# Optimization experiments

Hardware: AMD Instinct MI355X
Metric: run time of the kernel (lower is better)

The kernel has to match this reference:

```python
import jax, jax.numpy as jnp
import numpy as np

NUM_HEADS = 8
NEG_SLOPE = 0.2


def setup_inputs() -> dict:
    key = jax.random.key(0)
    k1, k2, k3, k4 = jax.random.split(key, 4)
    B, N, D_IN, D_K, D_V = 4, 4096, 256, 256, 256
    x = jax.random.normal(k1, (B, N, D_IN), dtype=jnp.float32)
    Wq = jax.random.normal(k2, (D_IN, D_K), dtype=jnp.float32) * (1.0 / np.sqrt(D_IN))
    Wk = jax.random.normal(k3, (D_IN, D_K), dtype=jnp.float32) * (1.0 / np.sqrt(D_IN))
    Wv = jax.random.normal(k4, (D_IN, D_V), dtype=jnp.float32) * (1.0 / np.sqrt(D_IN))
    return {"x": x, "Wq": Wq, "Wk": Wk, "Wv": Wv}


def reference(x, Wq, Wk, Wv):
    B, N, _ = x.shape
    nh = NUM_HEADS
    dim_k = Wq.shape[1]
    dim_v = Wv.shape[1]
    dk, dv = dim_k // nh, dim_v // nh
    nor_fact = 1.0 / np.sqrt(dk)
    # project and split heads: [B, H, N, dk]
    q = (x @ Wq).reshape(B, N, nh, dk).transpose(0, 2, 1, 3)
    k = (x @ Wk).reshape(B, N, nh, dk).transpose(0, 2, 1, 3)
    v = (x @ Wv).reshape(B, N, nh, dv).transpose(0, 2, 1, 3)
    # all-pairs scores, scaled then LeakyReLU (no softmax)
    dist = jnp.einsum('bhnd,bhmd->bhnm', q, k) * nor_fact
    dist = jnp.where(dist >= 0, dist, NEG_SLOPE * dist)
    att = jnp.einsum('bhnm,bhmd->bhnd', dist, v)
    return att.transpose(0, 2, 1, 3).reshape(B, N, dim_v)
```

## Files before the change

kernel.cpp:

```cpp
#include <hip/hip_runtime.h>

typedef __attribute__((ext_vector_type(8))) short short8;
typedef __attribute__((ext_vector_type(4))) float f32x4;
typedef __attribute__((ext_vector_type(2))) unsigned int u32x2;
typedef __attribute__((ext_vector_type(4))) unsigned int u32x4;

#define MFMA16x32(A, B, C) \
  __builtin_amdgcn_mfma_f32_16x16x32_bf16((A), (B), (C), 0, 0, 0)

__device__ __forceinline__ void async_cp16(const unsigned short* g, void* l) {
  __builtin_amdgcn_global_load_lds(
      (const __attribute__((address_space(1))) unsigned int*)g,
      (__attribute__((address_space(3))) unsigned int*)l, 16, 0, 0);
}

__device__ __forceinline__ unsigned int fbits(float f) {
  return __builtin_bit_cast(unsigned int, f);
}
__device__ __forceinline__ unsigned int pack_bf16(float a, float b) {
  return __builtin_amdgcn_perm(fbits(b), fbits(a), 0x07060302u);
}
__device__ __forceinline__ unsigned short bf16_rne(float f) {
  unsigned int u = fbits(f);
  return (unsigned short)((u + 0x8000u) >> 16);
}
__device__ __forceinline__ unsigned int relu_pk_bf16(unsigned int x) {
  unsigned int r;
  asm("v_pk_max_i16 %0, %1, 0" : "=v"(r) : "v"(x));
  return r;
}

__global__ __launch_bounds__(256) void prep_kernel(
    const float* __restrict__ x, unsigned short* __restrict__ xb,
    const float* __restrict__ Wq, const float* __restrict__ Wk,
    const float* __restrict__ Wv, unsigned short* __restrict__ WT) {
  __shared__ float tile[32][33];
  if (blockIdx.x < 4096) {
    const size_t i = ((size_t)blockIdx.x * 256 + threadIdx.x) * 4;
    const float4 f = *(const float4*)(x + i);
    u32x2 u = {(unsigned int)bf16_rne(f.x) | ((unsigned int)bf16_rne(f.y) << 16),
               (unsigned int)bf16_rne(f.z) | ((unsigned int)bf16_rne(f.w) << 16)};
    *(u32x2*)(xb + i) = u;
    return;
  }
  const int bid = blockIdx.x - 4096;
  const int g = bid / 64, rem = bid % 64;
  const int k0 = (rem >> 3) * 32, n0 = (rem & 7) * 32;
  const float* W = (g == 0) ? Wq : (g == 1) ? Wk : Wv;
  const int t = threadIdx.x;
  {
    const int kr = t >> 3, nc = (t & 7) * 4;
    const float4 f = *(const float4*)(W + (size_t)(k0 + kr) * 256 + n0 + nc);
    tile[kr][nc + 0] = f.x; tile[kr][nc + 1] = f.y;
    tile[kr][nc + 2] = f.z; tile[kr][nc + 3] = f.w;
  }
  __syncthreads();
  {
    const int nr = t >> 3, kc = (t & 7) * 4;
    unsigned int u0 = (unsigned int)bf16_rne(tile[kc + 0][nr]) |
                      ((unsigned int)bf16_rne(tile[kc + 1][nr]) << 16);
    unsigned int u1 = (unsigned int)bf16_rne(tile[kc + 2][nr]) |
                      ((unsigned int)bf16_rne(tile[kc + 3][nr]) << 16);
    u32x2 u = {u0, u1};
    *(u32x2*)(WT + (size_t)g * 65536 + (size_t)(n0 + nr) * 256 + k0 + kc) = u;
  }
}

__global__ __launch_bounds__(256, 2) void proj_kernel(
    const unsigned short* __restrict__ xb, const unsigned short* __restrict__ WT,
    unsigned short* __restrict__ QH, unsigned short* __restrict__ KH,
    unsigned short* __restrict__ VT) {
  __shared__ __align__(16) char smem[65536];
  const int tid = threadIdx.x;
  const int w = tid >> 6, lane = tid & 63, l15 = lane & 15, quad = lane >> 4;
  const int bid = blockIdx.x;
  const int mtile = bid / 6, nt = bid % 6;
  const int g = nt >> 1, n0 = (nt & 1) * 128;
  const int m0 = mtile * 128;

  const int srow = lane >> 3, useg = lane & 7;
  const int swz = (useg ^ srow) * 8;
  const unsigned short* aS = xb + (size_t)(m0 + w * 32 + srow) * 256 + swz;
  const unsigned short* bS =
      WT + (size_t)g * 65536 + (size_t)(n0 + w * 32 + srow) * 256 + swz;

#pragma unroll
  for (int j = 0; j < 4; j++) {
    async_cp16(aS + j * 2048, smem + w * 4096 + j * 1024);
    async_cp16(bS + j * 2048, smem + 16384 + w * 4096 + j * 1024);
  }
  __syncthreads();

  const f32x4 zero = {0.f, 0.f, 0.f, 0.f};
  f32x4 acc[2][8];
#pragma unroll
  for (int s = 0; s < 2; s++)
#pragma unroll
    for (int c = 0; c < 8; c++) acc[s][c] = zero;

  const int sw = l15 & 7;
  for (int t = 0; t < 4; t++) {
    const int nb = t & 1;
    const int kn = ((t + 1) & 3) * 64;
#pragma unroll
    for (int j = 0; j < 4; j++) {
      async_cp16(aS + kn + j * 2048,
                 smem + (nb ^ 1) * 32768 + w * 4096 + j * 1024);
      async_cp16(bS + kn + j * 2048,
                 smem + (nb ^ 1) * 32768 + 16384 + w * 4096 + j * 1024);
    }
    const char* Ab = smem + nb * 32768;
    const char* Bb = Ab + 16384;
#pragma unroll
    for (int ks = 0; ks < 2; ks++) {
      const int seg = ((ks * 4 + quad) ^ sw) * 16;
      short8 af[2], bf[8];
#pragma unroll
      for (int s = 0; s < 2; s++)
        af[s] = *(const short8*)(Ab + (w * 32 + s * 16 + l15) * 128 + seg);
#pragma unroll
      for (int c = 0; c < 8; c++)
        bf[c] = *(const short8*)(Bb + (c * 16 + l15) * 128 + seg);
      if (g < 2) {
#pragma unroll
        for (int s = 0; s < 2; s++)
#pragma unroll
          for (int c = 0; c < 8; c++)
            acc[s][c] = MFMA16x32(bf[c], af[s], acc[s][c]);
      } else {
#pragma unroll
        for (int s = 0; s < 2; s++)
#pragma unroll
          for (int c = 0; c < 8; c++)
            acc[s][c] = MFMA16x32(af[s], bf[c], acc[s][c]);
      }
    }
    __syncthreads();
  }

  if (g < 2) {
    unsigned short* O = g ? KH : QH;
    const float sc = g ? 1.0f : 0.17677669529663688f;
#pragma unroll
    for (int s = 0; s < 2; s++)
#pragma unroll
      for (int c = 0; c < 8; c++) {
        const int row = m0 + w * 32 + s * 16 + l15;
        const int col = n0 + c * 16 + quad * 4;
        const int bb = row >> 12, nn = row & 4095;
        const int hh = col >> 5, dl = col & 31;
        u32x2 pk = {pack_bf16(acc[s][c][0] * sc, acc[s][c][1] * sc),
                    pack_bf16(acc[s][c][2] * sc, acc[s][c][3] * sc)};
        *(u32x2*)(O + ((size_t)(bb * 8 + hh) * 4096 + nn) * 32 + dl) = pk;
      }
  } else {
#pragma unroll
    for (int s = 0; s < 2; s++)
#pragma unroll
      for (int c = 0; c < 8; c++) {
        const int col = n0 + c * 16 + l15;
        const int hh = col >> 5, dl = col & 31;
        const int row = m0 + w * 32 + s * 16 + quad * 4;
        const int bb = row >> 12;
        const int nn = (row & 4064) | (quad << 3) | ((s & 1) << 2);
        u32x2 pk = {pack_bf16(acc[s][c][0], acc[s][c][1]),
                    pack_bf16(acc[s][c][2], acc[s][c][3])};
        *(u32x2*)(VT + (size_t)((bb * 8 + hh) * 32 + dl) * 4096 + nn) = pk;
      }
  }
}

__global__ __launch_bounds__(512) void mkv_kernel(
    const unsigned short* __restrict__ KH, const unsigned short* __restrict__ VT,
    unsigned short* __restrict__ MW) {
  __shared__ __align__(16) float Mred[8][32][32];
  const int tid = threadIdx.x;
  const int w = tid >> 6, lane = tid & 63, l15 = lane & 15, quad = lane >> 4;
  const int bh = blockIdx.x;

  const f32x4 zero = {0.f, 0.f, 0.f, 0.f};
  f32x4 mm[2][2];
#pragma unroll
  for (int dt = 0; dt < 2; dt++)
#pragma unroll
    for (int it = 0; it < 2; it++) mm[dt][it] = zero;

  const unsigned short* Vg = VT + ((size_t)bh * 32 + l15) * 4096 + quad * 8;
  const unsigned short* Kg = KH + (size_t)bh * 4096 * 32;

  for (int g = 0; g < 16; g++) {
    const int kb = w * 512 + g * 32;
    short8 va[2];
#pragma unroll
    for (int dt = 0; dt < 2; dt++)
      va[dt] = *(const short8*)(Vg + (size_t)dt * 16 * 4096 + kb);
    short8 kv0, kv1;
#pragma unroll
    for (int j = 0; j < 8; j++) {
      const int key = kb + ((j >> 2) << 4) + quad * 4 + (j & 3);
      const size_t base = (size_t)key * 32 + l15;
      kv0[j] = (short)Kg[base];
      kv1[j] = (short)Kg[base + 16];
    }
#pragma unroll
    for (int dt = 0; dt < 2; dt++) {
      mm[dt][0] = MFMA16x32(va[dt], kv0, mm[dt][0]);
      mm[dt][1] = MFMA16x32(va[dt], kv1, mm[dt][1]);
    }
  }
#pragma unroll
  for (int dt = 0; dt < 2; dt++)
#pragma unroll
    for (int it = 0; it < 2; it++)
#pragma unroll
      for (int r = 0; r < 4; r++)
        Mred[w][dt * 16 + quad * 4 + r][it * 16 + l15] = mm[dt][it][r];
  __syncthreads();

  if (w == 0) {
#pragma unroll
    for (int dt = 0; dt < 2; dt++) {
      f32x4 sa = zero, sb = zero;
#pragma unroll
      for (int ww = 0; ww < 8; ww++) {
        const float* p = &Mred[ww][dt * 16 + l15][quad * 8];
        sa += *(const f32x4*)p;
        sb += *(const f32x4*)(p + 4);
      }
      u32x4 mw = {pack_bf16(sa[0], sa[1]), pack_bf16(sa[2], sa[3]),
                  pack_bf16(sb[0], sb[1]), pack_bf16(sb[2], sb[3])};
      *(u32x4*)(MW + (size_t)bh * 1024 + dt * 512 + lane * 8) = mw;
    }
  }
}

__global__ __launch_bounds__(512, 4) void attn_kernel(
    const unsigned short* __restrict__ QH, const unsigned short* __restrict__ KH,
    const unsigned short* __restrict__ VT, const unsigned short* __restrict__ MW,
    float* __restrict__ out) {
  __shared__ __align__(16) char smem[16384];
  const int tid = threadIdx.x;
  const int w = tid >> 6, lane = tid & 63, l15 = lane & 15, quad = lane >> 4;
  const int bid = blockIdx.x;
  const int bh = bid & 31, qh = bid >> 5;
  const int b = bh >> 3, h = bh & 7;
  const int qbase = qh * 256 + w * 32;

  const unsigned short* Qp =
      QH + ((size_t)bh * 4096 + qbase + l15) * 32 + quad * 8;
  short8 qf[2];
#pragma unroll
  for (int s = 0; s < 2; s++) qf[s] = *(const short8*)(Qp + (size_t)s * 512);

  short8 ma[2];
#pragma unroll
  for (int dt = 0; dt < 2; dt++)
    ma[dt] = *(const short8*)(MW + (size_t)bh * 1024 + dt * 512 + lane * 8);

  const bool isK = (w < 4);
  const unsigned short* src0;
  int kstr, wbOff;
  if (isK) {
    const int key = w * 16 + (lane >> 2);
    const int gseg = (lane & 3) ^ ((lane >> 3) & 3);
    src0 = KH + ((size_t)bh * 4096 + key) * 32 + gseg * 8;
    kstr = 32;
    wbOff = w * 1024;
  } else {
    const int r = (w - 4) * 8 + (lane >> 3), useg = lane & 7;
    src0 = VT + ((size_t)bh * 32 + r) * 4096 + ((useg ^ (r & 7)) * 8);
    kstr = 1;
    wbOff = 4096 + (w - 4) * 1024;
  }

  async_cp16(src0, smem + wbOff);
  __syncthreads();

  const f32x4 zero = {0.f, 0.f, 0.f, 0.f};
  f32x4 acc[2][2];
#pragma unroll
  for (int s = 0; s < 2; s++) {
    acc[s][0] = zero;
    acc[s][1] = zero;
  }

  const int rs = l15 & 7;
  const int kseg = (quad ^ ((l15 >> 1) & 3)) * 16;
  for (int i = 0; i < 64; i++) {
    const int nb = i & 1;
    const int kn = ((i + 1) & 63) * 64;
    async_cp16(src0 + (size_t)kn * kstr, smem + (nb ^ 1) * 8192 + wbOff);

    const char* Kb = smem + nb * 8192;
    const char* Vb = Kb + 4096;
    short8 kf[4];
#pragma unroll
    for (int c = 0; c < 4; c++)
      kf[c] = *(const short8*)(Kb + (c * 16 + l15) * 64 + kseg);
    short8 vf[2][2];
#pragma unroll
    for (int dt = 0; dt < 2; dt++) {
      const char* Vr = Vb + (dt * 16 + l15) * 128;
#pragma unroll
      for (int u = 0; u < 2; u++)
        vf[dt][u] = *(const short8*)(Vr + (((4 * u + quad) ^ rs) * 16));
    }

#pragma unroll
    for (int s = 0; s < 2; s++) {
      unsigned int pp[4][2];
#pragma unroll
      for (int c = 0; c < 4; c++) {
        f32x4 st = MFMA16x32(kf[c], qf[s], zero);
        pp[c][0] = relu_pk_bf16(pack_bf16(st[0], st[1]));
        pp[c][1] = relu_pk_bf16(pack_bf16(st[2], st[3]));
      }
#pragma unroll
      for (int u = 0; u < 2; u++) {
        u32x4 bw = {pp[2 * u][0], pp[2 * u][1],
                    pp[2 * u + 1][0], pp[2 * u + 1][1]};
        short8 pb = __builtin_bit_cast(short8, bw);
#pragma unroll
        for (int dt = 0; dt < 2; dt++)
          acc[s][dt] = MFMA16x32(vf[dt][u], pb, acc[s][dt]);
      }
    }
    __syncthreads();
  }

#pragma unroll
  for (int s = 0; s < 2; s++)
#pragma unroll
    for (int dt = 0; dt < 2; dt++) {
      f32x4 corr = MFMA16x32(ma[dt], qf[s], zero);
      f32x4 o = acc[s][dt] * 0.8f + corr * 0.2f;
      *(f32x4*)(out + ((size_t)b * 4096 + qbase + s * 16 + l15) * 256 + h * 32 +
                dt * 16 + quad * 4) = o;
    }
}

extern "C" void kernel_launch(void* const* d_in, const int* in_sizes, int n_in,
                              void* d_out, int out_size, void* d_ws,
                              size_t ws_size, hipStream_t stream) {
  const float* x = (const float*)d_in[0];
  const float* Wq = (const float*)d_in[1];
  const float* Wk = (const float*)d_in[2];
  const float* Wv = (const float*)d_in[3];
  float* out = (float*)d_out;

  unsigned short* ws = (unsigned short*)d_ws;
  unsigned short* QHb = ws;
  unsigned short* KHb = ws + 4194304;
  unsigned short* VTb = ws + 2 * 4194304;
  unsigned short* xbb = ws + 3 * 4194304;
  unsigned short* WTb = ws + 4 * 4194304;
  unsigned short* MWb = WTb + 196608;

  prep_kernel<<<4288, 256, 0, stream>>>(x, xbb, Wq, Wk, Wv, WTb);
  proj_kernel<<<768, 256, 0, stream>>>(xbb, WTb, QHb, KHb, VTb);
  mkv_kernel<<<32, 512, 0, stream>>>(KHb, VTb, MWb);
  attn_kernel<<<512, 512, 0, stream>>>(QHb, KHb, VTb, MWb, out);
}
```

Before: 155.2 us.

## Split mkv reduction across 8 key slices per head and reduce partials in attn

The mkv kernel previously ran only 32 blocks, each looping over all 4096 keys, which leaves most compute units idle. It now launches 256 blocks, each covering a 512-key slice, and writes fp32 partial M matrices. The attention kernel sums the 8 partials per head at startup and converts them to bf16. This trades a serial, underparallelised kernel for a little extra global traffic and redundant reduction work in every attention block.

```diff
diff --git a/kernel.cpp b/kernel.cpp
--- a/kernel.cpp
+++ b/kernel.cpp
@@ -172,11 +172,12 @@
 
 __global__ __launch_bounds__(512) void mkv_kernel(
     const unsigned short* __restrict__ KH, const unsigned short* __restrict__ VT,
-    unsigned short* __restrict__ MW) {
+    float* __restrict__ MP) {
   __shared__ __align__(16) float Mred[8][32][32];
   const int tid = threadIdx.x;
   const int w = tid >> 6, lane = tid & 63, l15 = lane & 15, quad = lane >> 4;
-  const int bh = blockIdx.x;
+  const int blk = blockIdx.x;
+  const int bh = blk >> 3, slice = blk & 7;
 
   const f32x4 zero = {0.f, 0.f, 0.f, 0.f};
   f32x4 mm[2][2];
@@ -188,8 +189,9 @@
   const unsigned short* Vg = VT + ((size_t)bh * 32 + l15) * 4096 + quad * 8;
   const unsigned short* Kg = KH + (size_t)bh * 4096 * 32;
 
-  for (int g = 0; g < 16; g++) {
-    const int kb = w * 512 + g * 32;
+#pragma unroll
+  for (int g = 0; g < 2; g++) {
+    const int kb = slice * 512 + w * 64 + g * 32;
     short8 va[2];
 #pragma unroll
     for (int dt = 0; dt < 2; dt++)
@@ -227,16 +229,16 @@
         sa += *(const f32x4*)p;
         sb += *(const f32x4*)(p + 4);
       }
-      u32x4 mw = {pack_bf16(sa[0], sa[1]), pack_bf16(sa[2], sa[3]),
-                  pack_bf16(sb[0], sb[1]), pack_bf16(sb[2], sb[3])};
-      *(u32x4*)(MW + (size_t)bh * 1024 + dt * 512 + lane * 8) = mw;
+      float* o = MP + (size_t)blk * 1024 + dt * 512 + lane * 8;
+      *(f32x4*)o = sa;
+      *(f32x4*)(o + 4) = sb;
     }
   }
 }
 
 __global__ __launch_bounds__(512, 4) void attn_kernel(
     const unsigned short* __restrict__ QH, const unsigned short* __restrict__ KH,
-    const unsigned short* __restrict__ VT, const unsigned short* __restrict__ MW,
+    const unsigned short* __restrict__ VT, const float* __restrict__ MP,
     float* __restrict__ out) {
   __shared__ __align__(16) char smem[16384];
   const int tid = threadIdx.x;
@@ -252,10 +254,34 @@
 #pragma unroll
   for (int s = 0; s < 2; s++) qf[s] = *(const short8*)(Qp + (size_t)s * 512);
 
+  const f32x4 zero = {0.f, 0.f, 0.f, 0.f};
+
   short8 ma[2];
-#pragma unroll
-  for (int dt = 0; dt < 2; dt++)
-    ma[dt] = *(const short8*)(MW + (size_t)bh * 1024 + dt * 512 + lane * 8);
+  {
+    f32x4 macc[2][2];
+#pragma unroll
+    for (int dt = 0; dt < 2; dt++) {
+      macc[dt][0] = zero;
+      macc[dt][1] = zero;
+    }
+#pragma unroll
+    for (int sl = 0; sl < 8; sl++) {
+      const float* p = MP + (size_t)(bh * 8 + sl) * 1024 + lane * 8;
+#pragma unroll
+      for (int dt = 0; dt < 2; dt++) {
+        macc[dt][0] += *(const f32x4*)(p + dt * 512);
+        macc[dt][1] += *(const f32x4*)(p + dt * 512 + 4);
+      }
+    }
+#pragma unroll
+    for (int dt = 0; dt < 2; dt++) {
+      u32x4 mw = {pack_bf16(macc[dt][0][0], macc[dt][0][1]),
+                  pack_bf16(macc[dt][0][2], macc[dt][0][3]),
+                  pack_bf16(macc[dt][1][0], macc[dt][1][1]),
+                  pack_bf16(macc[dt][1][2], macc[dt][1][3])};
+      ma[dt] = __builtin_bit_cast(short8, mw);
+    }
+  }
 
   const bool isK = (w < 4);
   const unsigned short* src0;
@@ -276,7 +302,6 @@
   async_cp16(src0, smem + wbOff);
   __syncthreads();
 
-  const f32x4 zero = {0.f, 0.f, 0.f, 0.f};
   f32x4 acc[2][2];
 #pragma unroll
   for (int s = 0; s < 2; s++) {
@@ -354,10 +379,10 @@
   unsigned short* VTb = ws + 2 * 4194304;
   unsigned short* xbb = ws + 3 * 4194304;
   unsigned short* WTb = ws + 4 * 4194304;
-  unsigned short* MWb = WTb + 196608;
+  float* MPf = (float*)(WTb + 196608);
 
   prep_kernel<<<4288, 256, 0, stream>>>(x, xbb, Wq, Wk, Wv, WTb);
   proj_kernel<<<768, 256, 0, stream>>>(xbb, WTb, QHb, KHb, VTb);
-  mkv_kernel<<<32, 512, 0, stream>>>(KHb, VTb, MWb);
-  attn_kernel<<<512, 512, 0, stream>>>(QHb, KHb, VTb, MWb, out);
-}
+  mkv_kernel<<<256, 512, 0, stream>>>(KHb, VTb, MPf);
+  attn_kernel<<<512, 512, 0, stream>>>(QHb, KHb, VTb, MPf, out);
+}
```

Result: slower. 168.1 us (+8.3%).

## Split K^T V reduction across eight blocks per head with separate reduce kernel

Applied to the files above, without the earlier changes.

The mkv kernel previously ran only 32 blocks, one per batch-head, each walking all 4096 keys, which leaves most CUs idle. It now launches 256 blocks, each covering a 512-key slice, and writes fp32 partial 32x32 matrices to workspace. A new small mred kernel sums the eight partials and packs them to bf16. This adds an extra launch and a small round trip of partials through global memory in exchange for higher parallelism.

```diff
diff --git a/kernel.cpp b/kernel.cpp
--- a/kernel.cpp
+++ b/kernel.cpp
@@ -172,11 +172,12 @@
 
 __global__ __launch_bounds__(512) void mkv_kernel(
     const unsigned short* __restrict__ KH, const unsigned short* __restrict__ VT,
-    unsigned short* __restrict__ MW) {
+    float* __restrict__ MP) {
   __shared__ __align__(16) float Mred[8][32][32];
   const int tid = threadIdx.x;
   const int w = tid >> 6, lane = tid & 63, l15 = lane & 15, quad = lane >> 4;
-  const int bh = blockIdx.x;
+  const int blk = blockIdx.x;
+  const int bh = blk >> 3, slice = blk & 7;
 
   const f32x4 zero = {0.f, 0.f, 0.f, 0.f};
   f32x4 mm[2][2];
@@ -188,8 +189,9 @@
   const unsigned short* Vg = VT + ((size_t)bh * 32 + l15) * 4096 + quad * 8;
   const unsigned short* Kg = KH + (size_t)bh * 4096 * 32;
 
-  for (int g = 0; g < 16; g++) {
-    const int kb = w * 512 + g * 32;
+#pragma unroll
+  for (int g = 0; g < 2; g++) {
+    const int kb = slice * 512 + w * 64 + g * 32;
     short8 va[2];
 #pragma unroll
     for (int dt = 0; dt < 2; dt++)
@@ -227,10 +229,31 @@
         sa += *(const f32x4*)p;
         sb += *(const f32x4*)(p + 4);
       }
-      u32x4 mw = {pack_bf16(sa[0], sa[1]), pack_bf16(sa[2], sa[3]),
-                  pack_bf16(sb[0], sb[1]), pack_bf16(sb[2], sb[3])};
-      *(u32x4*)(MW + (size_t)bh * 1024 + dt * 512 + lane * 8) = mw;
-    }
+      float* o = MP + (size_t)blk * 1024 + dt * 512 + lane * 8;
+      *(f32x4*)o = sa;
+      *(f32x4*)(o + 4) = sb;
+    }
+  }
+}
+
+__global__ __launch_bounds__(256) void mred_kernel(
+    const float* __restrict__ MP, unsigned short* __restrict__ MW) {
+  const int tid = threadIdx.x;
+  const int bh = blockIdx.x * 4 + (tid >> 6), lane = tid & 63;
+  const f32x4 zero = {0.f, 0.f, 0.f, 0.f};
+#pragma unroll
+  for (int dt = 0; dt < 2; dt++) {
+    f32x4 sa = zero, sb = zero;
+#pragma unroll
+    for (int sl = 0; sl < 8; sl++) {
+      const float* p =
+          MP + (size_t)(bh * 8 + sl) * 1024 + dt * 512 + lane * 8;
+      sa += *(const f32x4*)p;
+      sb += *(const f32x4*)(p + 4);
+    }
+    u32x4 mw = {pack_bf16(sa[0], sa[1]), pack_bf16(sa[2], sa[3]),
+                pack_bf16(sb[0], sb[1]), pack_bf16(sb[2], sb[3])};
+    *(u32x4*)(MW + (size_t)bh * 1024 + dt * 512 + lane * 8) = mw;
   }
 }
 
@@ -354,10 +377,12 @@
   unsigned short* VTb = ws + 2 * 4194304;
   unsigned short* xbb = ws + 3 * 4194304;
   unsigned short* WTb = ws + 4 * 4194304;
-  unsigned short* MWb = WTb + 196608;
+  float* MPf = (float*)(WTb + 196608);
+  unsigned short* MWb = (unsigned short*)(MPf + 262144);
 
   prep_kernel<<<4288, 256, 0, stream>>>(x, xbb, Wq, Wk, Wv, WTb);
   proj_kernel<<<768, 256, 0, stream>>>(xbb, WTb, QHb, KHb, VTb);
-  mkv_kernel<<<32, 512, 0, stream>>>(KHb, VTb, MWb);
+  mkv_kernel<<<256, 512, 0, stream>>>(KHb, VTb, MPf);
+  mred_kernel<<<8, 256, 0, stream>>>(MPf, MWb);
   attn_kernel<<<512, 512, 0, stream>>>(QHb, KHb, VTb, MWb, out);
 }
```

Result: no change. 153.3 us (-1.2%).
